# Optimization experiments

Hardware: AMD Instinct MI355X
Metric: run time of the kernel (lower is better)

The kernel has to match this reference:

```python
import jax, jax.numpy as jnp
import numpy as np

N = 10000      # nodes per QA graph
E = 128000     # edges per QA graph
A = 5          # answers (multiple choice)
D = 300        # glove embedding dim
H = 8          # heads layer 1
C1 = 64        # per-head out channels layer 1 (concat -> 512)
HID = 512
NEG_SLOPE = 0.2
EPS = 1e-16


def gat_layer(x, edge_index, W, a_src, a_dst, bias, concat):
    # x: [N, Din]; edge_index: [2, E]; W: [Din, H*C]; a_src/a_dst: [H, C]
    Hh, C = a_src.shape
    h = (x @ W).reshape(N, Hh, C)                      # transformed node feats
    alpha_src = (h * a_src[None]).sum(-1)              # [N, H]
    alpha_dst = (h * a_dst[None]).sum(-1)              # [N, H]
    src, dst = edge_index[0], edge_index[1]
    e = jax.nn.leaky_relu(alpha_src[src] + alpha_dst[dst], NEG_SLOPE)  # [E, H]
    # edge softmax grouped by destination node
    m = jax.ops.segment_max(e, dst, num_segments=N)    # [N, H]
    ex = jnp.exp(e - m[dst])
    denom = jax.ops.segment_sum(ex, dst, num_segments=N)
    alpha = ex / (denom[dst] + EPS)                    # [E, H]
    msg = alpha[:, :, None] * h[src]                   # [E, H, C]
    out = jax.ops.segment_sum(msg, dst, num_segments=N)  # [N, H, C]
    out = out.reshape(N, Hh * C) if concat else out.mean(axis=1)
    return out + bias, alpha


def setup_inputs() -> dict:
    key = jax.random.key(0)
    ks = jax.random.split(key, 10)
    s = 0.05
    return {
        "x": jax.random.normal(ks[0], (A, N, D), jnp.float32),
        "edge_index": jax.random.randint(ks[1], (A, 2, E), 0, N, dtype=jnp.int32),
        "W1": jax.random.normal(ks[2], (D, H * C1), jnp.float32) * s,
        "att_src1": jax.random.normal(ks[3], (H, C1), jnp.float32) * s,
        "att_dst1": jax.random.normal(ks[4], (H, C1), jnp.float32) * s,
        "bias1": jnp.zeros((H * C1,), jnp.float32),
        "W2": jax.random.normal(ks[5], (HID, 1), jnp.float32) * s,
        "att_src2": jax.random.normal(ks[6], (1, 1), jnp.float32) * s,
        "att_dst2": jax.random.normal(ks[7], (1, 1), jnp.float32) * s,
        "bias2": jnp.zeros((1,), jnp.float32),
    }


def reference(x, edge_index, W1, att_src1, att_dst1, bias1, W2, att_src2, att_dst2, bias2):
    def per_answer(xa, ei):
        h1, _ = gat_layer(xa, ei, W1, att_src1, att_dst1, bias1, concat=True)
        h1 = jax.nn.relu(h1)
        h2, alpha = gat_layer(h1, ei, W2, att_src2, att_dst2, bias2, concat=False)
        proba = h2.mean()                                  # scalar (x.mean(dim=0))
        # aggregate_attention: attention[dst] += edge_weight (edge_additive)
        att = jax.ops.segment_sum(alpha[:, 0], ei[1], num_segments=N)
        return proba, att

    proba_vec, atts = jax.vmap(per_answer)(x, edge_index)  # [A], [A, N]
    sel = atts[jnp.argmax(proba_vec)]                      # attentions[argmax]
    return proba_vec, sel
```

## Files before the change

kernel.cpp:

```cpp
#include <hip/hip_runtime.h>
#include <hip/hip_bf16.h>
#include <math.h>

#define NN 10000
#define EE 128000
#define AA 5
#define DD 300
#define HH 8
#define CC 64
#define HC 512
#define MM (AA*NN)
#define KP 320
#define NT (KP / 32)
#define NBM ((MM + 63) / 64)
#define SCB 40
#define SCN 250

typedef __attribute__((ext_vector_type(8))) _Float16 f16x8;
typedef __attribute__((ext_vector_type(4))) float f32x4;
typedef __attribute__((ext_vector_type(2))) float f32x2;
typedef unsigned short ushort;
typedef unsigned char uchar;

__device__ __forceinline__ ushort f2bf(float f) {
    unsigned u = __float_as_uint(f);
    unsigned r = u + 0x7fffu + ((u >> 16) & 1u);
    return (ushort)(r >> 16);
}
__device__ __forceinline__ float bf2f(ushort h) {
    return __uint_as_float(((unsigned)h) << 16);
}
__device__ __forceinline__ float leaky_exp(float v) {
    v = v > 0.f ? v : 0.2f * v;
    return __expf(v);
}


__global__ void count_edges(const int* __restrict__ ei, int* __restrict__ cnt) {
    int a = blockIdx.y;
    int e = blockIdx.x * 256 + threadIdx.x;
    if (e < EE) {
        int dst = ei[(size_t)a * 2 * EE + EE + e];
        atomicAdd(&cnt[a * NN + dst], 1);
    }
}


__global__ __launch_bounds__(256) void scan_bsum(const int* __restrict__ cnt,
                                                 int* __restrict__ bsum) {
    int a = blockIdx.y, b = blockIdx.x;
    int l = threadIdx.x;
    int v = (l < SCN) ? cnt[a * NN + b * SCN + l] : 0;
    #pragma unroll
    for (int o = 1; o < 64; o <<= 1) v += __shfl_xor(v, o);
    __shared__ int red[4];
    if ((l & 63) == 0) red[l >> 6] = v;
    __syncthreads();
    if (l == 0) bsum[a * SCB + b] = red[0] + red[1] + red[2] + red[3];
}

__global__ __launch_bounds__(64) void scan_bscan(const int* __restrict__ bsum,
                                                 int* __restrict__ boff,
                                                 int* __restrict__ offs) {
    int a = blockIdx.x;
    int l = threadIdx.x;
    int v = (l < SCB) ? bsum[a * SCB + l] : 0;
    int sc = v;
    #pragma unroll
    for (int o = 1; o < 64; o <<= 1) {
        int u = __shfl_up(sc, o);
        if (l >= o) sc += u;
    }
    if (l < SCB) boff[a * SCB + l] = sc - v;
    if (l == 63) offs[a * (NN + 1) + NN] = sc;
}

__global__ __launch_bounds__(256) void scan_final(const int* __restrict__ cnt,
                                                  const int* __restrict__ boff,
                                                  int* __restrict__ offs,
                                                  int* __restrict__ cursor) {
    int a = blockIdx.y, b = blockIdx.x;
    int l = threadIdx.x;
    int i = b * SCN + l;
    int v = (l < SCN) ? cnt[a * NN + i] : 0;
    int sc = v;
    int lane = l & 63, wv = l >> 6;
    #pragma unroll
    for (int o = 1; o < 64; o <<= 1) {
        int u = __shfl_up(sc, o);
        if (lane >= o) sc += u;
    }
    __shared__ int ws[4];
    if (lane == 63) ws[wv] = sc;
    __syncthreads();
    int woff = 0;
    #pragma unroll
    for (int w = 0; w < 4; ++w) woff += (w < wv) ? ws[w] : 0;
    if (l < SCN) {
        int o = boff[a * SCB + b] + woff + sc - v;
        offs[a * (NN + 1) + i] = o;
        cursor[a * (NN + 1) + i] = o;
    }
}

__global__ void scatter_edges(const int* __restrict__ ei, int* __restrict__ cursor,
                              int* __restrict__ csr_eid) {
    int a = blockIdx.y;
    int e = blockIdx.x * 256 + threadIdx.x;
    if (e < EE) {
        int dst = ei[(size_t)a * 2 * EE + EE + e];
        int pos = atomicAdd(&cursor[a * (NN + 1) + dst], 1);
        csr_eid[(size_t)a * EE + pos] = e;
    }
}


__global__ __launch_bounds__(256) void sort_src(const int* __restrict__ ei,
                                                const int* __restrict__ offs,
                                                int* __restrict__ csr_eid,
                                                int* __restrict__ csr_src,
                                                const float* __restrict__ asrc,
                                                const float* __restrict__ adst,
                                                float* __restrict__ w_csr) {
    int a = blockIdx.y;
    int wid = threadIdx.x >> 6, l = threadIdx.x & 63;
    int n = blockIdx.x * 4 + wid;
    if (n >= NN) return;
    const int* offsA = offs + a * (NN + 1);
    int beg = offsA[n], end = offsA[n + 1];
    int deg = end - beg;
    int* seg = csr_eid + (size_t)a * EE + beg;
    const int* srcrow = ei + (size_t)a * 2 * EE;
    const float* asrcA = asrc + (size_t)a * NN * HH;
    const float* adstA = adst + (size_t)a * NN * HH;
    float4 d0 = *(const float4*)(adstA + (size_t)n * HH);
    float4 d1 = *(const float4*)(adstA + (size_t)n * HH + 4);

    if (deg <= 64) {
        int v = (l < deg) ? seg[l] : 0x7fffffff;
        #pragma unroll
        for (int k = 2; k <= 64; k <<= 1)
            #pragma unroll
            for (int j = k >> 1; j > 0; j >>= 1) {
                int p = __shfl_xor(v, j);
                bool keepMin = (((l & k) == 0) == ((l & j) == 0));
                int mn = min(v, p), mx = max(v, p);
                v = keepMin ? mn : mx;
            }
        if (l < deg) {
            int s = srcrow[v];
            csr_src[(size_t)a * EE + beg + l] = s;
            float4 s0 = *(const float4*)(asrcA + (size_t)s * HH);
            float4 s1 = *(const float4*)(asrcA + (size_t)s * HH + 4);
            float4 w0, w1;
            w0.x = leaky_exp(s0.x + d0.x); w0.y = leaky_exp(s0.y + d0.y);
            w0.z = leaky_exp(s0.z + d0.z); w0.w = leaky_exp(s0.w + d0.w);
            w1.x = leaky_exp(s1.x + d1.x); w1.y = leaky_exp(s1.y + d1.y);
            w1.z = leaky_exp(s1.z + d1.z); w1.w = leaky_exp(s1.w + d1.w);
            float* wp = w_csr + ((size_t)a * EE + beg + l) * HH;
            *(float4*)(wp) = w0;
            *(float4*)(wp + 4) = w1;
        }
    } else {
        if (l == 0) {
            for (int i = 1; i < deg; ++i) {
                int key = seg[i];
                int j = i - 1;
                while (j >= 0 && seg[j] > key) { seg[j + 1] = seg[j]; --j; }
                seg[j + 1] = key;
            }
        }
        __builtin_amdgcn_wave_barrier();
        for (int i = l; i < deg; i += 64) {
            int s = srcrow[seg[i]];
            csr_src[(size_t)a * EE + beg + i] = s;
            float4 s0 = *(const float4*)(asrcA + (size_t)s * HH);
            float4 s1 = *(const float4*)(asrcA + (size_t)s * HH + 4);
            float4 w0, w1;
            w0.x = leaky_exp(s0.x + d0.x); w0.y = leaky_exp(s0.y + d0.y);
            w0.z = leaky_exp(s0.z + d0.z); w0.w = leaky_exp(s0.w + d0.w);
            w1.x = leaky_exp(s1.x + d1.x); w1.y = leaky_exp(s1.y + d1.y);
            w1.z = leaky_exp(s1.z + d1.z); w1.w = leaky_exp(s1.w + d1.w);
            float* wp = w_csr + ((size_t)a * EE + beg + i) * HH;
            *(float4*)(wp) = w0;
            *(float4*)(wp + 4) = w1;
        }
    }
}


__global__ __launch_bounds__(256) void pack_x(const float* __restrict__ X,
                                              ushort* __restrict__ Xp) {
    int gid = blockIdx.x * 256 + threadIdx.x;
    if (gid >= NBM * NT * 4 * 64) return;
    int l = gid & 63;
    int fr = (gid >> 6) & 3;
    int rest = gid >> 8;
    int ks = rest % NT;
    int bmi = rest / NT;
    int row = bmi * 64 + fr * 16 + (l & 15);
    int k = ks * 32 + (l >> 4) * 8;
    f16x8 o;
    if (row < MM && k + 8 <= DD) {
        float4 v0 = *(const float4*)(X + (size_t)row * DD + k);
        float4 v1 = *(const float4*)(X + (size_t)row * DD + k + 4);
        o[0] = (_Float16)v0.x; o[1] = (_Float16)v0.y;
        o[2] = (_Float16)v0.z; o[3] = (_Float16)v0.w;
        o[4] = (_Float16)v1.x; o[5] = (_Float16)v1.y;
        o[6] = (_Float16)v1.z; o[7] = (_Float16)v1.w;
    } else {
        #pragma unroll
        for (int j = 0; j < 8; ++j)
            o[j] = (row < MM && k + j < DD) ? (_Float16)X[(size_t)row * DD + k + j]
                                            : (_Float16)0.f;
    }
    *(f16x8*)(Xp + (size_t)gid * 8) = o;
}

__global__ __launch_bounds__(256) void pack_w(const float* __restrict__ W,
                                              ushort* __restrict__ Wp) {
    int gid = blockIdx.x * 256 + threadIdx.x;
    if (gid >= HH * NT * 4 * 64) return;
    int l = gid & 63;
    int fc = (gid >> 6) & 3;
    int rest = gid >> 8;
    int ks = rest % NT;
    int head = rest / NT;
    int col = head * 64 + fc * 16 + (l & 15);
    int k = ks * 32 + (l >> 4) * 8;
    f16x8 o;
    #pragma unroll
    for (int j = 0; j < 8; ++j)
        o[j] = (k + j < DD) ? (_Float16)W[(size_t)(k + j) * HC + col] : (_Float16)0.f;
    *(f16x8*)(Wp + (size_t)gid * 8) = o;
}


__global__ __launch_bounds__(256) void gemm_f16(const ushort* __restrict__ Xp,
                                                const ushort* __restrict__ Wp,
                                                const float* __restrict__ att_src1,
                                                const float* __restrict__ att_dst1,
                                                uchar* __restrict__ Hout,
                                                float* __restrict__ asrc,
                                                float* __restrict__ adst) {
    int wid = blockIdx.x * 4 + (threadIdx.x >> 6);
    int bmi = wid >> 3, head = wid & 7;
    if (bmi >= NBM) return;
    int bm = bmi * 64;
    int l = threadIdx.x & 63;
    int l16 = l & 15, kg = l >> 4;

    const ushort* Abase = Xp + (size_t)bmi * NT * 2048 + l * 8;
    const ushort* Bbase = Wp + (size_t)head * NT * 2048 + l * 8;

    f32x4 zz = {0.f, 0.f, 0.f, 0.f};
    f32x4 acc[4][4];
    #pragma unroll
    for (int i = 0; i < 4; ++i)
        #pragma unroll
        for (int j = 0; j < 4; ++j) acc[i][j] = zz;

    f16x8 aX[4], bX[4], aY[4], bY[4];
    #pragma unroll
    for (int f = 0; f < 4; ++f) {
        aX[f] = *(const f16x8*)(Abase + f * 512);
        bX[f] = *(const f16x8*)(Bbase + f * 512);
    }

    #pragma unroll
    for (int kk = 0; kk < NT; kk += 2) {
        if (kk + 1 < NT) {
            #pragma unroll
            for (int f = 0; f < 4; ++f) {
                aY[f] = *(const f16x8*)(Abase + (kk + 1) * 2048 + f * 512);
                bY[f] = *(const f16x8*)(Bbase + (kk + 1) * 2048 + f * 512);
            }
        }
        #pragma unroll
        for (int fr = 0; fr < 4; ++fr)
            #pragma unroll
            for (int fc = 0; fc < 4; ++fc)
                acc[fr][fc] = __builtin_amdgcn_mfma_f32_16x16x32_f16(aX[fr], bX[fc], acc[fr][fc], 0, 0, 0);
        if (kk + 2 < NT) {
            #pragma unroll
            for (int f = 0; f < 4; ++f) {
                aX[f] = *(const f16x8*)(Abase + (kk + 2) * 2048 + f * 512);
                bX[f] = *(const f16x8*)(Bbase + (kk + 2) * 2048 + f * 512);
            }
        }
        if (kk + 1 < NT) {
            #pragma unroll
            for (int fr = 0; fr < 4; ++fr)
                #pragma unroll
                for (int fc = 0; fc < 4; ++fc)
                    acc[fr][fc] = __builtin_amdgcn_mfma_f32_16x16x32_f16(aY[fr], bY[fc], acc[fr][fc], 0, 0, 0);
        }
    }

    float sv[4], dv[4];
    #pragma unroll
    for (int fc = 0; fc < 4; ++fc) {
        sv[fc] = att_src1[head * 64 + fc * 16 + l16];
        dv[fc] = att_dst1[head * 64 + fc * 16 + l16];
    }
    #pragma unroll
    for (int fr = 0; fr < 4; ++fr) {
        #pragma unroll
        for (int r = 0; r < 4; ++r) {
            int row = bm + fr * 16 + kg * 4 + r;
            bool ok = row < MM;
            float ps = 0.f, pd = 0.f;
            #pragma unroll
            for (int fc = 0; fc < 4; ++fc) {
                float val = acc[fr][fc][r];
                if (ok) {
                    int pk = __builtin_amdgcn_cvt_pk_fp8_f32(val, val, 0, false);
                    Hout[(size_t)row * HC + head * 64 + fc * 16 + l16] = (uchar)(pk & 0xff);
                }
                ps = fmaf(val, sv[fc], ps);
                pd = fmaf(val, dv[fc], pd);
            }
            #pragma unroll
            for (int o = 1; o < 16; o <<= 1) {
                ps += __shfl_xor(ps, o);
                pd += __shfl_xor(pd, o);
            }
            if (l16 == 0 && ok) {
                asrc[(size_t)row * HH + head] = ps;
                adst[(size_t)row * HH + head] = pd;
            }
        }
    }
}


__global__ __launch_bounds__(256) void layer1_agg(const uchar* __restrict__ h1,
                                                  const float* __restrict__ w_csr,
                                                  const int* __restrict__ offs,
                                                  const int* __restrict__ csr_src,
                                                  const float* __restrict__ bias1,
                                                  const float* __restrict__ W2,
                                                  float* __restrict__ h2) {
    int a = blockIdx.y;
    int wid = threadIdx.x >> 6, l = threadIdx.x & 63;
    int n = blockIdx.x * 4 + wid;
    int eg = l >> 3;
    int gh = l >> 3;

    const int* offsA = offs + a * (NN + 1);
    int beg = offsA[n], end = offsA[n + 1];
    int deg = end - beg;
    const int* srcs = csr_src + (size_t)a * EE + beg;
    const float* wA = w_csr + ((size_t)a * EE + beg) * HH;
    const uchar* h1A = h1 + (size_t)a * NN * HC;

    float denom = 0.f;
    float acc[8] = {};

    float w_cur = (eg < deg) ? wA[l] : 0.f;
    int s_cur = (eg < deg) ? srcs[eg] : 0;

    for (int c0 = 0; c0 < deg; c0 += 8) {
        float w_nxt = 0.f;
        int s_nxt = 0;
        if (c0 + 8 + eg < deg) {
            w_nxt = wA[(c0 + 8) * 8 + l];
            s_nxt = srcs[c0 + 8 + eg];
        }
        #pragma unroll
        for (int j = 0; j < 8; ++j) {
            if (c0 + j < deg) {
                float wj = __shfl(w_cur, j * 8 + gh);
                int sj = __shfl(s_cur, j * 8);
                uint2 hv = *(const uint2*)(h1A + (size_t)sj * HC + (l << 3));
                f32x2 p0 = __builtin_amdgcn_cvt_pk_f32_fp8((int)hv.x, false);
                f32x2 p1 = __builtin_amdgcn_cvt_pk_f32_fp8((int)hv.x, true);
                f32x2 p2 = __builtin_amdgcn_cvt_pk_f32_fp8((int)hv.y, false);
                f32x2 p3 = __builtin_amdgcn_cvt_pk_f32_fp8((int)hv.y, true);
                acc[0] = fmaf(wj, p0[0], acc[0]);
                acc[1] = fmaf(wj, p0[1], acc[1]);
                acc[2] = fmaf(wj, p1[0], acc[2]);
                acc[3] = fmaf(wj, p1[1], acc[3]);
                acc[4] = fmaf(wj, p2[0], acc[4]);
                acc[5] = fmaf(wj, p2[1], acc[5]);
                acc[6] = fmaf(wj, p3[0], acc[6]);
                acc[7] = fmaf(wj, p3[1], acc[7]);
            }
        }
        denom += w_cur;
        w_cur = w_nxt;
        s_cur = s_nxt;
    }
    #pragma unroll
    for (int o = 8; o < 64; o <<= 1) denom += __shfl_xor(denom, o);
    float dn = __shfl(denom, gh);
    float inv = 1.f / (dn + 1e-16f);

    int cb = l * 8;
    float4 b0 = *(const float4*)(bias1 + cb);
    float4 b1 = *(const float4*)(bias1 + cb + 4);
    float4 w0 = *(const float4*)(W2 + cb);
    float4 w1 = *(const float4*)(W2 + cb + 4);
    float bz[8] = {b0.x, b0.y, b0.z, b0.w, b1.x, b1.y, b1.z, b1.w};
    float wz[8] = {w0.x, w0.y, w0.z, w0.w, w1.x, w1.y, w1.z, w1.w};
    float p = 0.f;
    #pragma unroll
    for (int k = 0; k < 8; ++k) {
        float z = fmaf(acc[k], inv, bz[k]);
        z = z > 0.f ? z : 0.f;
        p = fmaf(z, wz[k], p);
    }
    #pragma unroll
    for (int o = 1; o < 64; o <<= 1) p += __shfl_xor(p, o);
    if (l == 0) h2[(size_t)a * NN + n] = p;
}


#define L2GRID 40

__global__ __launch_bounds__(256) void layer2_proba(const float* __restrict__ h2,
                                                    const int* __restrict__ offs,
                                                    const int* __restrict__ csr_src,
                                                    const float* __restrict__ att_src2,
                                                    const float* __restrict__ att_dst2,
                                                    const float* __restrict__ bias2,
                                                    float* __restrict__ partials) {
    int a = blockIdx.y;
    int n = blockIdx.x * 256 + threadIdx.x;
    float out2 = 0.f;
    if (n < NN) {
        const int* offsA = offs + a * (NN + 1);
        const int* srcs = csr_src + (size_t)a * EE;
        const float* h2A = h2 + (size_t)a * NN;
        float as2 = att_src2[0], ad2 = att_dst2[0];
        int beg = offsA[n], end = offsA[n + 1];
        float adn = h2A[n] * ad2;
        float denom = 0.f, accv = 0.f;
        for (int i = beg; i < end; ++i) {
            float hs = h2A[srcs[i]];
            float v = fmaf(hs, as2, adn);
            v = v > 0.f ? v : 0.2f * v;
            float w = __expf(v);
            denom += w;
            accv = fmaf(w, hs, accv);
        }
        out2 = accv / (denom + 1e-16f) + bias2[0];
    }
    __shared__ float red[256];
    red[threadIdx.x] = out2;
    __syncthreads();
    for (int s = 128; s > 0; s >>= 1) {
        if (threadIdx.x < s) red[threadIdx.x] += red[threadIdx.x + s];
        __syncthreads();
    }
    if (threadIdx.x == 0) partials[a * L2GRID + blockIdx.x] = red[0];
}

__global__ __launch_bounds__(256) void finalize_proba(const float* __restrict__ partials,
                                                      float* __restrict__ out,
                                                      int* __restrict__ best) {
    int tid = threadIdx.x;
    __shared__ float red[256];
    red[tid] = (tid < AA * L2GRID) ? partials[tid] : 0.f;
    __syncthreads();
    if (tid == 0) {
        float pv[AA];
        for (int a = 0; a < AA; ++a) {
            float s = 0.f;
            for (int i = 0; i < L2GRID; ++i) s += red[a * L2GRID + i];
            pv[a] = s / (float)NN;
            out[a] = pv[a];
        }
        int b = 0;
        for (int a = 1; a < AA; ++a)
            if (pv[a] > pv[b]) b = a;
        *best = b;
    }
}

__global__ void write_sel(const int* __restrict__ cnt, const int* __restrict__ best,
                          float* __restrict__ out) {
    int n = blockIdx.x * 256 + threadIdx.x;
    if (n < NN) out[AA + n] = (cnt[(*best) * NN + n] > 0) ? 1.0f : 0.0f;
}


extern "C" void kernel_launch(void* const* d_in, const int* in_sizes, int n_in,
                              void* d_out, int out_size, void* d_ws, size_t ws_size,
                              hipStream_t stream) {
    const float* x        = (const float*)d_in[0];
    const int*   ei       = (const int*)d_in[1];
    const float* W1       = (const float*)d_in[2];
    const float* att_src1 = (const float*)d_in[3];
    const float* att_dst1 = (const float*)d_in[4];
    const float* bias1    = (const float*)d_in[5];
    const float* W2       = (const float*)d_in[6];
    const float* att_src2 = (const float*)d_in[7];
    const float* att_dst2 = (const float*)d_in[8];
    const float* bias2    = (const float*)d_in[9];
    float* out = (float*)d_out;

    char* ws = (char*)d_ws;
    size_t off = 0;
    auto alloc = [&](size_t bytes) {
        size_t cur = off;
        off += (bytes + 255) & ~(size_t)255;
        return cur;
    };
    uchar*  h1      = (uchar*)(ws + alloc(sizeof(uchar) * (size_t)MM * HC));
    ushort* xp      = (ushort*)(ws + alloc(sizeof(ushort) * (size_t)NBM * NT * 2048));
    float*  asrc    = (float*)(ws + alloc(sizeof(float) * (size_t)MM * HH));
    float*  adst    = (float*)(ws + alloc(sizeof(float) * (size_t)MM * HH));
    float*  h2      = (float*)(ws + alloc(sizeof(float) * (size_t)MM));
    int*    cnt     = (int*)(ws + alloc(sizeof(int) * (size_t)AA * NN));
    int*    offs    = (int*)(ws + alloc(sizeof(int) * (size_t)AA * (NN + 1)));
    int*    cursor  = (int*)(ws + alloc(sizeof(int) * (size_t)AA * (NN + 1)));
    int*    bsum    = (int*)(ws + alloc(sizeof(int) * (size_t)AA * SCB));
    int*    boff    = (int*)(ws + alloc(sizeof(int) * (size_t)AA * SCB));
    int*    csr_eid = (int*)(ws + alloc(sizeof(int) * (size_t)AA * EE));
    int*    csr_src = (int*)(ws + alloc(sizeof(int) * (size_t)AA * EE));
    float*  w_csr   = (float*)(ws + alloc(sizeof(float) * (size_t)AA * EE * HH));
    float*  partials= (float*)(ws + alloc(sizeof(float) * AA * L2GRID));
    int*    best    = (int*)(ws + alloc(sizeof(int) * 16));
    ushort* wp      = (ushort*)(ws + alloc(sizeof(ushort) * (size_t)HH * NT * 2048));
    (void)ws_size; (void)in_sizes; (void)n_in; (void)out_size;

    pack_w<<<dim3((HH * NT * 256 + 255) / 256), dim3(256), 0, stream>>>(W1, wp);
    pack_x<<<dim3((NBM * NT * 256 + 255) / 256), dim3(256), 0, stream>>>(x, xp);

    hipMemsetAsync(cnt, 0, sizeof(int) * (size_t)AA * NN, stream);
    count_edges<<<dim3(EE / 256, AA), dim3(256), 0, stream>>>(ei, cnt);
    scan_bsum<<<dim3(SCB, AA), dim3(256), 0, stream>>>(cnt, bsum);
    scan_bscan<<<dim3(AA), dim3(64), 0, stream>>>(bsum, boff, offs);
    scan_final<<<dim3(SCB, AA), dim3(256), 0, stream>>>(cnt, boff, offs, cursor);
    scatter_edges<<<dim3(EE / 256, AA), dim3(256), 0, stream>>>(ei, cursor, csr_eid);

    gemm_f16<<<dim3((NBM * 8 + 3) / 4), dim3(256), 0, stream>>>(
        xp, wp, att_src1, att_dst1, h1, asrc, adst);

    sort_src<<<dim3(NN / 4, AA), dim3(256), 0, stream>>>(ei, offs, csr_eid, csr_src,
                                                         asrc, adst, w_csr);

    layer1_agg<<<dim3(NN / 4, AA), dim3(256), 0, stream>>>(h1, w_csr, offs, csr_src,
                                                           bias1, W2, h2);

    layer2_proba<<<dim3(L2GRID, AA), dim3(256), 0, stream>>>(h2, offs, csr_src,
                                                             att_src2, att_dst2, bias2,
                                                             partials);

    finalize_proba<<<dim3(1), dim3(256), 0, stream>>>(partials, out, best);
    write_sel<<<dim3((NN + 255) / 256), dim3(256), 0, stream>>>(cnt, best, out);
}
```

Baseline: 235.9 us.

## Fuse edge scatter with attention weight computation and drop per-node sort

Replaces the separate scatter_edges and sort_src kernels with one edge-parallel kernel. It atomically claims a CSR slot, writes the source index and computes the eight leaky-exp attention weights directly. This removes the csr_eid buffer, one launch, and the per-destination bitonic/insertion sort, including the serial insertion sort for high-degree nodes. The trade-off is that edge order within each destination segment becomes nondeterministic, so float summation order in aggregation can vary from run to run. Reads of the asrc/adst rows are now random per edge instead of grouped by destination.

```diff
diff --git a/kernel.cpp b/kernel.cpp
--- a/kernel.cpp
+++ b/kernel.cpp
@@ -103,89 +103,34 @@
     }
 }
 
-__global__ void scatter_edges(const int* __restrict__ ei, int* __restrict__ cursor,
-                              int* __restrict__ csr_eid) {
+
+__global__ __launch_bounds__(256) void scatter_fused(const int* __restrict__ ei,
+                                                     int* __restrict__ cursor,
+                                                     int* __restrict__ csr_src,
+                                                     const float* __restrict__ asrc,
+                                                     const float* __restrict__ adst,
+                                                     float* __restrict__ w_csr) {
     int a = blockIdx.y;
     int e = blockIdx.x * 256 + threadIdx.x;
-    if (e < EE) {
-        int dst = ei[(size_t)a * 2 * EE + EE + e];
-        int pos = atomicAdd(&cursor[a * (NN + 1) + dst], 1);
-        csr_eid[(size_t)a * EE + pos] = e;
-    }
-}
-
-
-__global__ __launch_bounds__(256) void sort_src(const int* __restrict__ ei,
-                                                const int* __restrict__ offs,
-                                                int* __restrict__ csr_eid,
-                                                int* __restrict__ csr_src,
-                                                const float* __restrict__ asrc,
-                                                const float* __restrict__ adst,
-                                                float* __restrict__ w_csr) {
-    int a = blockIdx.y;
-    int wid = threadIdx.x >> 6, l = threadIdx.x & 63;
-    int n = blockIdx.x * 4 + wid;
-    if (n >= NN) return;
-    const int* offsA = offs + a * (NN + 1);
-    int beg = offsA[n], end = offsA[n + 1];
-    int deg = end - beg;
-    int* seg = csr_eid + (size_t)a * EE + beg;
-    const int* srcrow = ei + (size_t)a * 2 * EE;
+    if (e >= EE) return;
+    int src = ei[(size_t)a * 2 * EE + e];
+    int dst = ei[(size_t)a * 2 * EE + EE + e];
+    int pos = atomicAdd(&cursor[a * (NN + 1) + dst], 1);
+    csr_src[(size_t)a * EE + pos] = src;
     const float* asrcA = asrc + (size_t)a * NN * HH;
     const float* adstA = adst + (size_t)a * NN * HH;
-    float4 d0 = *(const float4*)(adstA + (size_t)n * HH);
-    float4 d1 = *(const float4*)(adstA + (size_t)n * HH + 4);
-
-    if (deg <= 64) {
-        int v = (l < deg) ? seg[l] : 0x7fffffff;
-        #pragma unroll
-        for (int k = 2; k <= 64; k <<= 1)
-            #pragma unroll
-            for (int j = k >> 1; j > 0; j >>= 1) {
-                int p = __shfl_xor(v, j);
-                bool keepMin = (((l & k) == 0) == ((l & j) == 0));
-                int mn = min(v, p), mx = max(v, p);
-                v = keepMin ? mn : mx;
-            }
-        if (l < deg) {
-            int s = srcrow[v];
-            csr_src[(size_t)a * EE + beg + l] = s;
-            float4 s0 = *(const float4*)(asrcA + (size_t)s * HH);
-            float4 s1 = *(const float4*)(asrcA + (size_t)s * HH + 4);
-            float4 w0, w1;
-            w0.x = leaky_exp(s0.x + d0.x); w0.y = leaky_exp(s0.y + d0.y);
-            w0.z = leaky_exp(s0.z + d0.z); w0.w = leaky_exp(s0.w + d0.w);
-            w1.x = leaky_exp(s1.x + d1.x); w1.y = leaky_exp(s1.y + d1.y);
-            w1.z = leaky_exp(s1.z + d1.z); w1.w = leaky_exp(s1.w + d1.w);
-            float* wp = w_csr + ((size_t)a * EE + beg + l) * HH;
-            *(float4*)(wp) = w0;
-            *(float4*)(wp + 4) = w1;
-        }
-    } else {
-        if (l == 0) {
-            for (int i = 1; i < deg; ++i) {
-                int key = seg[i];
-                int j = i - 1;
-                while (j >= 0 && seg[j] > key) { seg[j + 1] = seg[j]; --j; }
-                seg[j + 1] = key;
-            }
-        }
-        __builtin_amdgcn_wave_barrier();
-        for (int i = l; i < deg; i += 64) {
-            int s = srcrow[seg[i]];
-            csr_src[(size_t)a * EE + beg + i] = s;
-            float4 s0 = *(const float4*)(asrcA + (size_t)s * HH);
-            float4 s1 = *(const float4*)(asrcA + (size_t)s * HH + 4);
-            float4 w0, w1;
-            w0.x = leaky_exp(s0.x + d0.x); w0.y = leaky_exp(s0.y + d0.y);
-            w0.z = leaky_exp(s0.z + d0.z); w0.w = leaky_exp(s0.w + d0.w);
-            w1.x = leaky_exp(s1.x + d1.x); w1.y = leaky_exp(s1.y + d1.y);
-            w1.z = leaky_exp(s1.z + d1.z); w1.w = leaky_exp(s1.w + d1.w);
-            float* wp = w_csr + ((size_t)a * EE + beg + i) * HH;
-            *(float4*)(wp) = w0;
-            *(float4*)(wp + 4) = w1;
-        }
-    }
+    float4 s0 = *(const float4*)(asrcA + (size_t)src * HH);
+    float4 s1 = *(const float4*)(asrcA + (size_t)src * HH + 4);
+    float4 d0 = *(const float4*)(adstA + (size_t)dst * HH);
+    float4 d1 = *(const float4*)(adstA + (size_t)dst * HH + 4);
+    float4 w0, w1;
+    w0.x = leaky_exp(s0.x + d0.x); w0.y = leaky_exp(s0.y + d0.y);
+    w0.z = leaky_exp(s0.z + d0.z); w0.w = leaky_exp(s0.w + d0.w);
+    w1.x = leaky_exp(s1.x + d1.x); w1.y = leaky_exp(s1.y + d1.y);
+    w1.z = leaky_exp(s1.z + d1.z); w1.w = leaky_exp(s1.w + d1.w);
+    float* wp = w_csr + ((size_t)a * EE + pos) * HH;
+    *(float4*)(wp) = w0;
+    *(float4*)(wp + 4) = w1;
 }
 
 
@@ -517,7 +462,6 @@
     int*    cursor  = (int*)(ws + alloc(sizeof(int) * (size_t)AA * (NN + 1)));
     int*    bsum    = (int*)(ws + alloc(sizeof(int) * (size_t)AA * SCB));
     int*    boff    = (int*)(ws + alloc(sizeof(int) * (size_t)AA * SCB));
-    int*    csr_eid = (int*)(ws + alloc(sizeof(int) * (size_t)AA * EE));
     int*    csr_src = (int*)(ws + alloc(sizeof(int) * (size_t)AA * EE));
     float*  w_csr   = (float*)(ws + alloc(sizeof(float) * (size_t)AA * EE * HH));
     float*  partials= (float*)(ws + alloc(sizeof(float) * AA * L2GRID));
@@ -533,13 +477,12 @@
     scan_bsum<<<dim3(SCB, AA), dim3(256), 0, stream>>>(cnt, bsum);
     scan_bscan<<<dim3(AA), dim3(64), 0, stream>>>(bsum, boff, offs);
     scan_final<<<dim3(SCB, AA), dim3(256), 0, stream>>>(cnt, boff, offs, cursor);
-    scatter_edges<<<dim3(EE / 256, AA), dim3(256), 0, stream>>>(ei, cursor, csr_eid);
 
     gemm_f16<<<dim3((NBM * 8 + 3) / 4), dim3(256), 0, stream>>>(
         xp, wp, att_src1, att_dst1, h1, asrc, adst);
 
-    sort_src<<<dim3(NN / 4, AA), dim3(256), 0, stream>>>(ei, offs, csr_eid, csr_src,
-                                                         asrc, adst, w_csr);
+    scatter_fused<<<dim3(EE / 256, AA), dim3(256), 0, stream>>>(ei, cursor, csr_src,
+                                                                asrc, adst, w_csr);
 
     layer1_agg<<<dim3(NN / 4, AA), dim3(256), 0, stream>>>(h1, w_csr, offs, csr_src,
                                                            bias1, W2, h2);
```

After: 221.0 us. -6.3%, faster.
